# Kernel tuning notes

Hardware: AMD Instinct MI355X
Metric: run time of the kernel (lower is better)

## Reference

```python
import jax, jax.numpy as jnp
import numpy as np
from jax import lax

K = 16
SIGMA2 = 1.0  # sigma=1.0 squared
EPS = 1e-06


def setup_inputs() -> dict:
    key = jax.random.key(0)
    xyz = jax.random.normal(key, (4, 3, 4096), dtype=jnp.float32)
    return {"xyz": xyz}


def reference(xyz):
    # xyz: (B, 3, N)
    B, _, N = xyz.shape
    pts = jnp.transpose(xyz, (0, 2, 1))  # (B, N, 3)

    sq = jnp.sum(pts * pts, axis=-1)  # (B, N)
    d2 = sq[:, :, None] + sq[:, None, :] - 2.0 * jnp.einsum("bnd,bmd->bnm", pts, pts)

    # k nearest neighbors (smallest distance, includes self like torch knn on same set)
    _, idx = lax.top_k(-d2, K)  # idx: (B, N, K)

    # gather neighbor coordinates and recompute exact squared distance (faithful to source)
    neighbors = jax.vmap(lambda p, i: p[i])(pts, idx)  # (B, N, K, 3)
    diff = pts[:, :, None, :] - neighbors
    dist2 = jnp.sum(diff * diff, axis=-1)  # (B, N, K)
    weights = jnp.exp(-dist2 / (2.0 * SIGMA2))

    # scatter k-sparse weights into dense adjacency (topk indices per row are unique)
    bb = jnp.arange(B)[:, None, None]
    ii = jnp.arange(N)[None, :, None]
    A = jnp.zeros((B, N, N), dtype=xyz.dtype).at[bb, ii, idx].set(weights)
    A = 0.5 * (A + jnp.swapaxes(A, 1, 2))

    # symmetric normalized Laplacian L = I - D^{-1/2} A D^{-1/2} (diag scaling via broadcast)
    D = jnp.clip(jnp.sum(A, axis=-1), EPS, None)
    d_is = D ** -0.5  # (B, N)
    L = jnp.eye(N, dtype=xyz.dtype)[None] - d_is[:, :, None] * A * d_is[:, None, :]
    return L
```

## Files before the change

### kernel.cpp

```cpp
#include <hip/hip_runtime.h>
#include <math.h>

#pragma clang fp contract(off)

#define NPTS 4096
#define KNN  16
#define RPBK 16
#define KT   1024
#define CAP  128
#define CAPIN 64
#define SPILLCAP 262144

__device__ __forceinline__ unsigned okey(float f) {
    f = f + 0.0f;
    unsigned u = __float_as_uint(f);
    return u ^ (((unsigned)((int)u >> 31)) | 0x80000000u);
}

__device__ __forceinline__ unsigned wmin32(unsigned v) {
    for (int o = 32; o > 0; o >>= 1) { unsigned w = __shfl_xor(v, o); v = w < v ? w : v; }
    return v;
}
__device__ __forceinline__ unsigned long long wmin64(unsigned long long v) {
    for (int o = 32; o > 0; o >>= 1) { unsigned long long w = __shfl_xor(v, o); v = w < v ? w : v; }
    return v;
}

__global__ void zero_kernel(float* __restrict__ p, int n) {
    int i = blockIdx.x * blockDim.x + threadIdx.x;
    if (i < n) p[i] = 0.0f;
}

__global__ __launch_bounds__(KT, 8) void knn_kernel(const float* __restrict__ xyz,
                                                    float* __restrict__ Dsum,
                                                    int* __restrict__ idx_out,
                                                    float* __restrict__ w_out,
                                                    int* __restrict__ cnt,
                                                    int* __restrict__ inc,
                                                    int* __restrict__ spillc,
                                                    int* __restrict__ spill,
                                                    int do_inc) {
    __shared__ float4 spts[NPTS];
    __shared__ int    lists[RPBK][CAP];

    const int t    = threadIdx.x;
    const int lane = t & 63;
    const int wv   = t >> 6;
    const int rowg = blockIdx.x * RPBK + wv;
    const int b    = rowg >> 12;
    const float* X = xyz + (size_t)b * 3 * NPTS;

    for (int i = t; i < NPTS; i += KT) {
        float x = X[i], y = X[NPTS + i], z = X[2 * NPTS + i];
        spts[i] = make_float4(x, y, z, (x * x + y * y) + z * z);
    }
    __syncthreads();

    const float4 P = spts[rowg & (NPTS - 1)];

    unsigned best1 = 0xFFFFFFFFu;
    for (int i = 0; i < NPTS / 64; ++i) {
        float4 Q  = spts[i * 64 + lane];
        float dot = (P.x * Q.x + P.y * Q.y) + P.z * Q.z;
        float d2  = (P.w + Q.w) - 2.0f * dot;
        unsigned k = okey(d2);
        best1 = k < best1 ? k : best1;
    }
    unsigned cur = best1, T = 0;
    for (int r = 0; r < KNN; ++r) {
        unsigned mn = wmin32(cur);
        T = mn;
        if (cur == mn) cur = 0xFFFFFFFFu;
    }

    int cnt2 = 0;
    for (int i = 0; i < NPTS / 64; ++i) {
        int m = i * 64 + lane;
        float4 Q  = spts[m];
        float dot = (P.x * Q.x + P.y * Q.y) + P.z * Q.z;
        float d2  = (P.w + Q.w) - 2.0f * dot;
        bool pass = okey(d2) <= T;
        unsigned long long bal = __ballot(pass);
        if (pass) {
            int pos = cnt2 + __popcll(bal & ((1ull << lane) - 1ull));
            if (pos < CAP) lists[wv][pos] = m;
        }
        cnt2 += (int)__popcll(bal);
    }

    unsigned long long sel = ~0ull;
    if (cnt2 <= CAP) {
        unsigned long long e0 = ~0ull, e1 = ~0ull;
        if (lane < cnt2) {
            int m = lists[wv][lane]; float4 Q = spts[m];
            float dot = (P.x * Q.x + P.y * Q.y) + P.z * Q.z;
            float d2  = (P.w + Q.w) - 2.0f * dot;
            e0 = ((unsigned long long)okey(d2) << 32) | (unsigned)m;
        }
        if (lane + 64 < cnt2) {
            int m = lists[wv][lane + 64]; float4 Q = spts[m];
            float dot = (P.x * Q.x + P.y * Q.y) + P.z * Q.z;
            float d2  = (P.w + Q.w) - 2.0f * dot;
            e1 = ((unsigned long long)okey(d2) << 32) | (unsigned)m;
        }
        unsigned long long c = e0 < e1 ? e0 : e1;
        for (int r = 0; r < KNN; ++r) {
            unsigned long long mn = wmin64(c);
            if (c == mn) {
                if (e0 == mn) e0 = ~0ull; else e1 = ~0ull;
                c = e0 < e1 ? e0 : e1;
            }
            if (lane == r) sel = mn;
        }
    } else {
        unsigned long long last = 0;
        for (int r = 0; r < KNN; ++r) {
            unsigned long long bestp = ~0ull;
            for (int i = 0; i < NPTS / 64; ++i) {
                int m = i * 64 + lane;
                float4 Q  = spts[m];
                float dot = (P.x * Q.x + P.y * Q.y) + P.z * Q.z;
                float d2  = (P.w + Q.w) - 2.0f * dot;
                unsigned long long key = ((unsigned long long)okey(d2) << 32) | (unsigned)m;
                if (key > last && key < bestp) bestp = key;
            }
            unsigned long long mn = wmin64(bestp);
            if (lane == r) sel = mn;
            last = mn;
        }
    }

    float wgt = 0.0f;
    if (lane < KNN) {
        int j = (int)(unsigned)(sel & 0xFFFFFFFFull);
        float4 Q = spts[j];
        float dx = P.x - Q.x, dy = P.y - Q.y, dz = P.z - Q.z;
        float dist2 = (dx * dx + dy * dy) + dz * dz;
        wgt = expf(-(dist2 * 0.5f));
        size_t base = (size_t)rowg * KNN + lane;
        idx_out[base] = j;
        w_out[base]   = wgt;
        int jg = (b << 12) + j;
        atomicAdd(&Dsum[jg], 0.5f * wgt);
        if (do_inc) {
            int pos = atomicAdd(&cnt[jg], 1);
            if (pos < CAPIN) {
                inc[(size_t)jg * CAPIN + pos] = (int)base;
            } else {
                int sp = atomicAdd(spillc, 1);
                if (sp < SPILLCAP) spill[sp] = (int)base;
            }
        }
    }
    float rs = wgt;
    for (int o = 32; o > 0; o >>= 1) rs += __shfl_xor(rs, o);
    if (lane == 0) atomicAdd(&Dsum[rowg], 0.5f * rs);
}

__global__ void dis_kernel(const float* __restrict__ Dsum, float* __restrict__ dis, int n) {
    int i = blockIdx.x * blockDim.x + threadIdx.x;
    if (i < n) dis[i] = 1.0f / sqrtf(fmaxf(Dsum[i], 1e-6f));
}

__global__ __launch_bounds__(256) void row_kernel(const int* __restrict__ idxb,
                                                  const float* __restrict__ wb,
                                                  const float* __restrict__ dis,
                                                  const int* __restrict__ cnt,
                                                  const int* __restrict__ inc,
                                                  float* __restrict__ L) {
    __shared__ float row[NPTS];
    const int r = blockIdx.x;
    const int b = r >> 12;
    const int n = r & (NPTS - 1);

    float4* row4 = (float4*)row;
    for (int i = threadIdx.x; i < NPTS / 4; i += 256)
        row4[i] = make_float4(0.0f, 0.0f, 0.0f, 0.0f);
    __syncthreads();

    const float dn = dis[r];

    if (threadIdx.x < KNN) {
        int g = r * KNN + threadIdx.x;
        int j = idxb[g];
        float v = -0.5f * wb[g] * dn * dis[(b << 12) + j];
        atomicAdd(&row[j], v);
    }

    int c = cnt[r];
    if (c > CAPIN) c = CAPIN;
    for (int i = threadIdx.x; i < c; i += 256) {
        int g   = inc[(size_t)r * CAPIN + i];
        int src = g >> 4;
        float v = -0.5f * wb[g] * dis[src] * dn;
        atomicAdd(&row[src & (NPTS - 1)], v);
    }
    __syncthreads();

    float4* Lr = (float4*)(L + (size_t)b * NPTS * NPTS + (size_t)n * NPTS);
    const int dq = n >> 2, dl = n & 3;
    for (int i = threadIdx.x; i < NPTS / 4; i += 256) {
        float4 v = row4[i];
        if (i == dq) ((float*)&v)[dl] += 1.0f;
        Lr[i] = v;
    }
}

__global__ __launch_bounds__(256) void spill_kernel(const int* __restrict__ spillc,
                                                    const int* __restrict__ spill,
                                                    const int* __restrict__ idxb,
                                                    const float* __restrict__ wb,
                                                    const float* __restrict__ dis,
                                                    float* __restrict__ L) {
    int c = spillc[0];
    if (c > SPILLCAP) c = SPILLCAP;
    for (int i = blockIdx.x * blockDim.x + threadIdx.x; i < c;
         i += gridDim.x * blockDim.x) {
        int g   = spill[i];
        int src = g >> 4;
        int b   = src >> 12;
        int nn  = src & (NPTS - 1);
        int j   = idxb[g];
        float v = -0.5f * wb[g] * dis[src] * dis[(b << 12) + j];
        atomicAdd(L + (size_t)b * NPTS * NPTS + (size_t)j * NPTS + nn, v);
    }
}

__global__ __launch_bounds__(256) void fill_kernel(float4* __restrict__ L4, size_t T4) {
    size_t g4     = (size_t)blockIdx.x * blockDim.x + threadIdx.x;
    size_t stride = (size_t)gridDim.x * blockDim.x;
    for (; g4 < T4; g4 += stride) {
        size_t g = g4 << 2;
        int o    = (int)(g & (size_t)(NPTS * (size_t)NPTS - 1));
        int row  = o >> 12;
        int col0 = o & (NPTS - 1);
        float4 v;
        v.x = (row == col0    ) ? 1.0f : 0.0f;
        v.y = (row == col0 + 1) ? 1.0f : 0.0f;
        v.z = (row == col0 + 2) ? 1.0f : 0.0f;
        v.w = (row == col0 + 3) ? 1.0f : 0.0f;
        L4[g4] = v;
    }
}

__global__ __launch_bounds__(256) void scatter_kernel(const int* __restrict__ idxb,
                                                      const float* __restrict__ wb,
                                                      const float* __restrict__ dis,
                                                      float* __restrict__ L) {
    int g   = blockIdx.x * 256 + threadIdx.x;
    int row = g >> 4;
    int b   = row >> 12;
    int n   = row & (NPTS - 1);
    int j   = idxb[g];
    float v = -0.5f * wb[g] * dis[row] * dis[(b << 12) + j];
    float* Lb = L + (size_t)b * NPTS * NPTS;
    atomicAdd(Lb + (size_t)n * NPTS + j, v);
    atomicAdd(Lb + (size_t)j * NPTS + n, v);
}

extern "C" void kernel_launch(void* const* d_in, const int* in_sizes, int n_in,
                              void* d_out, int out_size, void* d_ws, size_t ws_size,
                              hipStream_t stream) {
    const float* xyz = (const float*)d_in[0];
    const int B  = in_sizes[0] / (3 * NPTS);
    const int BN = B * NPTS;

    float* Dsum   = (float*)d_ws;
    int*   cnt    = (int*)(Dsum + BN);
    int*   spillc = cnt + BN;
    float* dis    = (float*)(spillc + 16);
    int*   idxb   = (int*)(dis + BN);
    float* wb     = (float*)(idxb + (size_t)BN * KNN);
    int*   inc    = (int*)(wb + (size_t)BN * KNN);
    int*   spill  = inc + (size_t)BN * CAPIN;
    float* L      = (float*)d_out;

    size_t need = ((size_t)BN * (3 + 2 * KNN + CAPIN) + 16 + SPILLCAP) * 4;
    const int fused = (ws_size >= need);

    if (fused) {
        int nz = 2 * BN + 16;
        zero_kernel<<<(nz + 255) / 256, 256, 0, stream>>>(Dsum, nz);
        knn_kernel<<<BN / RPBK, KT, 0, stream>>>(xyz, Dsum, idxb, wb,
                                                 cnt, inc, spillc, spill, 1);
        dis_kernel<<<BN / 256, 256, 0, stream>>>(Dsum, dis, BN);
        row_kernel<<<BN, 256, 0, stream>>>(idxb, wb, dis, cnt, inc, L);
        spill_kernel<<<64, 256, 0, stream>>>(spillc, spill, idxb, wb, dis, L);
    } else {
        float* fDsum = (float*)d_ws;
        float* fdis  = fDsum + BN;
        int*   fidx  = (int*)(fdis + BN);
        float* fwb   = (float*)(fidx + (size_t)BN * KNN);
        zero_kernel<<<BN / 256, 256, 0, stream>>>(fDsum, BN);
        knn_kernel<<<BN / RPBK, KT, 0, stream>>>(xyz, fDsum, fidx, fwb,
                                                 nullptr, nullptr, nullptr, nullptr, 0);
        dis_kernel<<<BN / 256, 256, 0, stream>>>(fDsum, fdis, BN);
        size_t T4 = (size_t)B * NPTS * NPTS / 4;
        fill_kernel<<<8192, 256, 0, stream>>>((float4*)d_out, T4);
        scatter_kernel<<<(BN * KNN) / 256, 256, 0, stream>>>(fidx, fwb, fdis, L);
    }
}
```

Measured before the change: 378.1 us.

## Process two query rows per wave in kNN and two rows per Laplacian block

The kNN kernel now has each wave handle two query rows, so every shared-memory point load is reused for two distance computations. The 16th-smallest threshold and the final selection for small candidate lists now use a float rank-by-shuffle instead of repeated wave-min reductions. The row kernel writes two output rows per 512-thread block to cut the block count. Costs are higher register pressure, larger per-block shared memory, and half as many kNN blocks.

```diff
diff --git a/kernel.cpp b/kernel.cpp
--- a/kernel.cpp
+++ b/kernel.cpp
@@ -5,11 +5,12 @@
 
 #define NPTS 4096
 #define KNN  16
-#define RPBK 16
+#define RPBK 32
 #define KT   1024
 #define CAP  128
 #define CAPIN 64
 #define SPILLCAP 262144
+#define RROWS 2
 
 __device__ __forceinline__ unsigned okey(float f) {
     f = f + 0.0f;
@@ -17,10 +18,6 @@
     return u ^ (((unsigned)((int)u >> 31)) | 0x80000000u);
 }
 
-__device__ __forceinline__ unsigned wmin32(unsigned v) {
-    for (int o = 32; o > 0; o >>= 1) { unsigned w = __shfl_xor(v, o); v = w < v ? w : v; }
-    return v;
-}
 __device__ __forceinline__ unsigned long long wmin64(unsigned long long v) {
     for (int o = 32; o > 0; o >>= 1) { unsigned long long w = __shfl_xor(v, o); v = w < v ? w : v; }
     return v;
@@ -31,78 +28,50 @@
     if (i < n) p[i] = 0.0f;
 }
 
-__global__ __launch_bounds__(KT, 8) void knn_kernel(const float* __restrict__ xyz,
-                                                    float* __restrict__ Dsum,
-                                                    int* __restrict__ idx_out,
-                                                    float* __restrict__ w_out,
-                                                    int* __restrict__ cnt,
-                                                    int* __restrict__ inc,
-                                                    int* __restrict__ spillc,
-                                                    int* __restrict__ spill,
-                                                    int do_inc) {
-    __shared__ float4 spts[NPTS];
-    __shared__ int    lists[RPBK][CAP];
-
-    const int t    = threadIdx.x;
-    const int lane = t & 63;
-    const int wv   = t >> 6;
-    const int rowg = blockIdx.x * RPBK + wv;
-    const int b    = rowg >> 12;
-    const float* X = xyz + (size_t)b * 3 * NPTS;
-
-    for (int i = t; i < NPTS; i += KT) {
-        float x = X[i], y = X[NPTS + i], z = X[2 * NPTS + i];
-        spts[i] = make_float4(x, y, z, (x * x + y * y) + z * z);
-    }
-    __syncthreads();
-
-    const float4 P = spts[rowg & (NPTS - 1)];
-
-    unsigned best1 = 0xFFFFFFFFu;
-    for (int i = 0; i < NPTS / 64; ++i) {
-        float4 Q  = spts[i * 64 + lane];
-        float dot = (P.x * Q.x + P.y * Q.y) + P.z * Q.z;
-        float d2  = (P.w + Q.w) - 2.0f * dot;
-        unsigned k = okey(d2);
-        best1 = k < best1 ? k : best1;
-    }
-    unsigned cur = best1, T = 0;
-    for (int r = 0; r < KNN; ++r) {
-        unsigned mn = wmin32(cur);
-        T = mn;
-        if (cur == mn) cur = 0xFFFFFFFFu;
-    }
-
-    int cnt2 = 0;
-    for (int i = 0; i < NPTS / 64; ++i) {
-        int m = i * 64 + lane;
-        float4 Q  = spts[m];
-        float dot = (P.x * Q.x + P.y * Q.y) + P.z * Q.z;
-        float d2  = (P.w + Q.w) - 2.0f * dot;
-        bool pass = okey(d2) <= T;
-        unsigned long long bal = __ballot(pass);
-        if (pass) {
-            int pos = cnt2 + __popcll(bal & ((1ull << lane) - 1ull));
-            if (pos < CAP) lists[wv][pos] = m;
-        }
-        cnt2 += (int)__popcll(bal);
-    }
-
-    unsigned long long sel = ~0ull;
-    if (cnt2 <= CAP) {
+__device__ __forceinline__ float thresh16(float k, int lane) {
+    int rank = 0;
+    for (int s = 0; s < 64; ++s) {
+        float ks = __shfl(k, s);
+        rank += (ks < k || (ks == k && s < lane)) ? 1 : 0;
+    }
+    unsigned long long m = __ballot(rank == 15);
+    return __shfl(k, __ffsll(m) - 1);
+}
+
+__device__ __forceinline__ int select16(const float4* __restrict__ spts,
+                                        const int* __restrict__ list,
+                                        int cnt, float4 P, int lane) {
+    if (cnt <= 64) {
+        float key = __builtin_huge_valf();
+        int m = -1;
+        if (lane < cnt) {
+            m = list[lane];
+            float4 Q = spts[m];
+            float dot = (P.x * Q.x + P.y * Q.y) + P.z * Q.z;
+            key = (P.w + Q.w) - 2.0f * dot;
+        }
+        int rank = 0;
+        for (int s = 0; s < 64; ++s) {
+            float ks = __shfl(key, s);
+            rank += (ks < key || (ks == key && s < lane)) ? 1 : 0;
+        }
+        return __builtin_amdgcn_ds_permute(rank << 2, m);
+    }
+    if (cnt <= CAP) {
         unsigned long long e0 = ~0ull, e1 = ~0ull;
-        if (lane < cnt2) {
-            int m = lists[wv][lane]; float4 Q = spts[m];
+        if (lane < cnt) {
+            int m = list[lane]; float4 Q = spts[m];
             float dot = (P.x * Q.x + P.y * Q.y) + P.z * Q.z;
             float d2  = (P.w + Q.w) - 2.0f * dot;
             e0 = ((unsigned long long)okey(d2) << 32) | (unsigned)m;
         }
-        if (lane + 64 < cnt2) {
-            int m = lists[wv][lane + 64]; float4 Q = spts[m];
+        if (lane + 64 < cnt) {
+            int m = list[lane + 64]; float4 Q = spts[m];
             float dot = (P.x * Q.x + P.y * Q.y) + P.z * Q.z;
             float d2  = (P.w + Q.w) - 2.0f * dot;
             e1 = ((unsigned long long)okey(d2) << 32) | (unsigned)m;
         }
+        int selm = -1;
         unsigned long long c = e0 < e1 ? e0 : e1;
         for (int r = 0; r < KNN; ++r) {
             unsigned long long mn = wmin64(c);
@@ -110,29 +79,41 @@
                 if (e0 == mn) e0 = ~0ull; else e1 = ~0ull;
                 c = e0 < e1 ? e0 : e1;
             }
-            if (lane == r) sel = mn;
-        }
-    } else {
-        unsigned long long last = 0;
-        for (int r = 0; r < KNN; ++r) {
-            unsigned long long bestp = ~0ull;
-            for (int i = 0; i < NPTS / 64; ++i) {
-                int m = i * 64 + lane;
-                float4 Q  = spts[m];
-                float dot = (P.x * Q.x + P.y * Q.y) + P.z * Q.z;
-                float d2  = (P.w + Q.w) - 2.0f * dot;
-                unsigned long long key = ((unsigned long long)okey(d2) << 32) | (unsigned)m;
-                if (key > last && key < bestp) bestp = key;
-            }
-            unsigned long long mn = wmin64(bestp);
-            if (lane == r) sel = mn;
-            last = mn;
-        }
-    }
-
+            if (lane == r) selm = (int)(unsigned)(mn & 0xFFFFFFFFull);
+        }
+        return selm;
+    }
+    unsigned long long last = 0; int selm = -1;
+    for (int r = 0; r < KNN; ++r) {
+        unsigned long long bestp = ~0ull;
+        for (int i = 0; i < NPTS / 64; ++i) {
+            int m = i * 64 + lane;
+            float4 Q  = spts[m];
+            float dot = (P.x * Q.x + P.y * Q.y) + P.z * Q.z;
+            float d2  = (P.w + Q.w) - 2.0f * dot;
+            unsigned long long key = ((unsigned long long)okey(d2) << 32) | (unsigned)m;
+            if (key > last && key < bestp) bestp = key;
+        }
+        unsigned long long mn = wmin64(bestp);
+        if (lane == r) selm = (int)(unsigned)(mn & 0xFFFFFFFFull);
+        last = mn;
+    }
+    return selm;
+}
+
+__device__ __forceinline__ void emit_row(int rowg, int b, int selm, float4 P,
+                                         const float4* __restrict__ spts,
+                                         float* __restrict__ Dsum,
+                                         int* __restrict__ idx_out,
+                                         float* __restrict__ w_out,
+                                         int* __restrict__ cnt,
+                                         int* __restrict__ inc,
+                                         int* __restrict__ spillc,
+                                         int* __restrict__ spill,
+                                         int do_inc, int lane) {
     float wgt = 0.0f;
     if (lane < KNN) {
-        int j = (int)(unsigned)(sel & 0xFFFFFFFFull);
+        int j = selm;
         float4 Q = spts[j];
         float dx = P.x - Q.x, dy = P.y - Q.y, dz = P.z - Q.z;
         float dist2 = (dx * dx + dy * dy) + dz * dz;
@@ -157,52 +138,131 @@
     if (lane == 0) atomicAdd(&Dsum[rowg], 0.5f * rs);
 }
 
+__global__ __launch_bounds__(KT, 8) void knn_kernel(const float* __restrict__ xyz,
+                                                    float* __restrict__ Dsum,
+                                                    int* __restrict__ idx_out,
+                                                    float* __restrict__ w_out,
+                                                    int* __restrict__ cnt,
+                                                    int* __restrict__ inc,
+                                                    int* __restrict__ spillc,
+                                                    int* __restrict__ spill,
+                                                    int do_inc) {
+    __shared__ float4 spts[NPTS];
+    __shared__ int    lists[RPBK][CAP];
+
+    const int t    = threadIdx.x;
+    const int lane = t & 63;
+    const int wv   = t >> 6;
+    const int row0 = blockIdx.x * RPBK + 2 * wv;
+    const int b    = row0 >> 12;
+    const float* X = xyz + (size_t)b * 3 * NPTS;
+
+    for (int i = t; i < NPTS; i += KT) {
+        float x = X[i], y = X[NPTS + i], z = X[2 * NPTS + i];
+        spts[i] = make_float4(x, y, z, (x * x + y * y) + z * z);
+    }
+    __syncthreads();
+
+    const float4 PA = spts[row0 & (NPTS - 1)];
+    const float4 PB = spts[(row0 + 1) & (NPTS - 1)];
+
+    float bA = __builtin_huge_valf(), bB = __builtin_huge_valf();
+    for (int i = 0; i < NPTS / 64; ++i) {
+        float4 Q  = spts[i * 64 + lane];
+        float dotA = (PA.x * Q.x + PA.y * Q.y) + PA.z * Q.z;
+        float d2A  = (PA.w + Q.w) - 2.0f * dotA;
+        float dotB = (PB.x * Q.x + PB.y * Q.y) + PB.z * Q.z;
+        float d2B  = (PB.w + Q.w) - 2.0f * dotB;
+        bA = fminf(bA, d2A);
+        bB = fminf(bB, d2B);
+    }
+    const float TA = thresh16(bA, lane);
+    const float TB = thresh16(bB, lane);
+
+    int* listA = &lists[2 * wv][0];
+    int* listB = &lists[2 * wv + 1][0];
+    int cA = 0, cB = 0;
+    for (int i = 0; i < NPTS / 64; ++i) {
+        int m = i * 64 + lane;
+        float4 Q  = spts[m];
+        float dotA = (PA.x * Q.x + PA.y * Q.y) + PA.z * Q.z;
+        float d2A  = (PA.w + Q.w) - 2.0f * dotA;
+        float dotB = (PB.x * Q.x + PB.y * Q.y) + PB.z * Q.z;
+        float d2B  = (PB.w + Q.w) - 2.0f * dotB;
+        bool pA = d2A <= TA;
+        unsigned long long balA = __ballot(pA);
+        if (pA) {
+            int pos = cA + __popcll(balA & ((1ull << lane) - 1ull));
+            if (pos < CAP) listA[pos] = m;
+        }
+        cA += (int)__popcll(balA);
+        bool pB = d2B <= TB;
+        unsigned long long balB = __ballot(pB);
+        if (pB) {
+            int pos = cB + __popcll(balB & ((1ull << lane) - 1ull));
+            if (pos < CAP) listB[pos] = m;
+        }
+        cB += (int)__popcll(balB);
+    }
+
+    int selA = select16(spts, listA, cA, PA, lane);
+    int selB = select16(spts, listB, cB, PB, lane);
+    emit_row(row0,     b, selA, PA, spts, Dsum, idx_out, w_out,
+             cnt, inc, spillc, spill, do_inc, lane);
+    emit_row(row0 + 1, b, selB, PB, spts, Dsum, idx_out, w_out,
+             cnt, inc, spillc, spill, do_inc, lane);
+}
+
 __global__ void dis_kernel(const float* __restrict__ Dsum, float* __restrict__ dis, int n) {
     int i = blockIdx.x * blockDim.x + threadIdx.x;
     if (i < n) dis[i] = 1.0f / sqrtf(fmaxf(Dsum[i], 1e-6f));
 }
 
-__global__ __launch_bounds__(256) void row_kernel(const int* __restrict__ idxb,
+__global__ __launch_bounds__(512) void row_kernel(const int* __restrict__ idxb,
                                                   const float* __restrict__ wb,
                                                   const float* __restrict__ dis,
                                                   const int* __restrict__ cnt,
                                                   const int* __restrict__ inc,
                                                   float* __restrict__ L) {
-    __shared__ float row[NPTS];
-    const int r = blockIdx.x;
-    const int b = r >> 12;
-    const int n = r & (NPTS - 1);
+    __shared__ float row[RROWS * NPTS];
+    const int r0 = blockIdx.x * RROWS;
+    const int b  = r0 >> 12;
 
     float4* row4 = (float4*)row;
-    for (int i = threadIdx.x; i < NPTS / 4; i += 256)
+    for (int i = threadIdx.x; i < RROWS * NPTS / 4; i += 512)
         row4[i] = make_float4(0.0f, 0.0f, 0.0f, 0.0f);
     __syncthreads();
 
+    const int rr = threadIdx.x >> 8;
+    const int tt = threadIdx.x & 255;
+    const int r  = r0 + rr;
+    float* myrow = row + rr * NPTS;
     const float dn = dis[r];
 
-    if (threadIdx.x < KNN) {
-        int g = r * KNN + threadIdx.x;
+    if (tt < KNN) {
+        int g = r * KNN + tt;
         int j = idxb[g];
         float v = -0.5f * wb[g] * dn * dis[(b << 12) + j];
-        atomicAdd(&row[j], v);
+        atomicAdd(&myrow[j], v);
     }
 
     int c = cnt[r];
     if (c > CAPIN) c = CAPIN;
-    for (int i = threadIdx.x; i < c; i += 256) {
+    for (int i = tt; i < c; i += 256) {
         int g   = inc[(size_t)r * CAPIN + i];
         int src = g >> 4;
         float v = -0.5f * wb[g] * dis[src] * dn;
-        atomicAdd(&row[src & (NPTS - 1)], v);
+        atomicAdd(&myrow[src & (NPTS - 1)], v);
     }
     __syncthreads();
 
-    float4* Lr = (float4*)(L + (size_t)b * NPTS * NPTS + (size_t)n * NPTS);
-    const int dq = n >> 2, dl = n & 3;
-    for (int i = threadIdx.x; i < NPTS / 4; i += 256) {
-        float4 v = row4[i];
-        if (i == dq) ((float*)&v)[dl] += 1.0f;
-        Lr[i] = v;
+    const int n0 = r0 & (NPTS - 1);
+    float4* Lr = (float4*)(L + (size_t)b * NPTS * NPTS + (size_t)n0 * NPTS);
+    for (int q = threadIdx.x; q < RROWS * NPTS / 4; q += 512) {
+        float4 v = row4[q];
+        int n = n0 + (q >> 10);
+        if ((q & 1023) == (n >> 2)) ((float*)&v)[n & 3] += 1.0f;
+        Lr[q] = v;
     }
 }
 
@@ -284,7 +344,7 @@
         knn_kernel<<<BN / RPBK, KT, 0, stream>>>(xyz, Dsum, idxb, wb,
                                                  cnt, inc, spillc, spill, 1);
         dis_kernel<<<BN / 256, 256, 0, stream>>>(Dsum, dis, BN);
-        row_kernel<<<BN, 256, 0, stream>>>(idxb, wb, dis, cnt, inc, L);
+        row_kernel<<<BN / RROWS, 512, 0, stream>>>(idxb, wb, dis, cnt, inc, L);
         spill_kernel<<<64, 256, 0, stream>>>(spillc, spill, idxb, wb, dis, L);
     } else {
         float* fDsum = (float*)d_ws;
```

New measurement: 344.9 us. 8.8% less time.
